# Kernel optimization log

Measured on AMD Instinct MI355X. Metric: run time of the kernel, lower is better.

## Reference

```python
import jax, jax.numpy as jnp
import numpy as np

MIN_NORM = 1e-15
PROJ_EPS = 4e-3   # HGCN fp32 boundary eps
C = 1.0           # curvature (args.c)
SQRT_C = 1.0
LOOP_ATT = 10.0   # self-loop weight


def _norm(x):
    return jnp.clip(jnp.linalg.norm(x, axis=-1, keepdims=True), MIN_NORM)


def artanh(x):
    x = jnp.clip(x, -1.0 + 1e-6, 1.0 - 1e-6)
    return 0.5 * (jnp.log1p(x) - jnp.log1p(-x))


def proj(x):
    # project back inside the Poincare ball
    n = _norm(x)
    maxn = (1.0 - PROJ_EPS) / SQRT_C
    return jnp.where(n > maxn, x / n * maxn, x)


def expmap0(u):
    n = _norm(u)
    return jnp.tanh(SQRT_C * n) * u / (SQRT_C * n)


def logmap0(p):
    n = _norm(p)
    return artanh(SQRT_C * n) * p / (SQRT_C * n)


def mobius_add(x, y):
    x2 = jnp.sum(x * x, -1, keepdims=True)
    y2 = jnp.sum(y * y, -1, keepdims=True)
    xy = jnp.sum(x * y, -1, keepdims=True)
    num = (1.0 + 2.0 * C * xy + C * y2) * x + (1.0 - C * x2) * y
    den = 1.0 + 2.0 * C * xy + C * C * x2 * y2
    return num / jnp.clip(den, MIN_NORM)


def mobius_matvec(W, x):
    xn = _norm(x)
    mx = x @ W.T                       # [N, out]
    mxn = _norm(mx)
    res = jnp.tanh(mxn / xn * artanh(SQRT_C * xn)) * mx / (mxn * SQRT_C)
    zero = jnp.all(mx == 0, axis=-1, keepdims=True)
    return jnp.where(zero, 0.0, res)


def normalize_adj(adj):
    # symmetric D^{-1/2} A D^{-1/2}
    deg = jnp.sum(adj, axis=-1)
    dinv = jnp.where(deg > 0, deg ** -0.5, 0.0)
    return dinv[:, None] * adj * dinv[None, :]


def encode(x, adj, W_stack, b_stack):
    # map features onto the manifold: proj(expmap0(proj_tan0(x))) ; proj_tan0 = id
    h = proj(expmap0(x))
    for i in range(W_stack.shape[0]):
        # HypLinear: mobius matvec + hyperbolic bias add
        m = proj(mobius_matvec(W_stack[i], h))
        hb = proj(expmap0(b_stack[i][None, :]))
        m = proj(mobius_add(m, hb))
        # HypAgg: aggregate in tangent space at origin
        m = proj(expmap0(adj @ logmap0(m)))
        # HypAct: relu in tangent space
        h = proj(expmap0(jax.nn.relu(logmap0(m))))
    return h


def readout(h):
    # cat(global_avg_pool, global_max_pool) over nodes -> [2*d]
    return jnp.concatenate([jnp.mean(h, axis=0), jnp.max(h, axis=0)])


def setup_inputs() -> dict:
    key = jax.random.key(0)
    ks = jax.random.split(key, 12)
    N, F, D, L = 4096, 128, 128, 2
    x1 = jax.random.normal(ks[0], (1, N, F), jnp.float32)
    x2 = jax.random.normal(ks[1], (1, N, F), jnp.float32)
    adj1 = jax.random.uniform(ks[2], (1, N, N), dtype=jnp.float32)
    adj2 = jax.random.uniform(ks[3], (1, N, N), dtype=jnp.float32)
    dist1 = jax.random.uniform(ks[4], (N, N), dtype=jnp.float32)
    dist2 = jax.random.uniform(ks[5], (N, N), dtype=jnp.float32)
    W_stack = jax.random.normal(ks[6], (L, D, F), jnp.float32) * 0.05
    b_stack = jax.random.normal(ks[7], (L, D), jnp.float32) * 0.01
    W_mlp1 = jax.random.normal(ks[8], (D, 6 * D), jnp.float32) * 0.05
    b_mlp1 = jnp.zeros((D,), jnp.float32)
    W_mlp2 = jax.random.normal(ks[9], (1, D), jnp.float32) * 0.05
    b_mlp2 = jnp.zeros((1,), jnp.float32)
    return dict(x1=x1, x2=x2, adj1=adj1, adj2=adj2, dist1=dist1, dist2=dist2,
                W_stack=W_stack, b_stack=b_stack,
                W_mlp1=W_mlp1, b_mlp1=b_mlp1, W_mlp2=W_mlp2, b_mlp2=b_mlp2)


def reference(x1, x2, adj1, adj2, dist1, dist2, W_stack, b_stack,
              W_mlp1, b_mlp1, W_mlp2, b_mlp2):
    N = x1.shape[1]
    eye = jnp.eye(N, dtype=x1.dtype)
    a1 = normalize_adj(adj1[0] + LOOP_ATT * eye)
    a2 = normalize_adj(adj2[0] + LOOP_ATT * eye)
    out1 = encode(x1[0], a1, W_stack, b_stack)
    out2 = encode(x2[0], a2, W_stack, b_stack)
    h1 = readout(out1)
    h2 = readout(out2)
    feat = jnp.concatenate([h1, h2, h1 - h2])            # [6*d]
    hidden = jax.nn.gelu(feat @ W_mlp1.T + b_mlp1, approximate=False)
    logits = hidden @ W_mlp2.T + b_mlp2                  # [1]
    return logits
```

## Files before the change

kernel.cpp:

```cpp
#include <hip/hip_runtime.h>
#include <math.h>

#define MIN_NORM 1e-15f
#define MAXN 0.996f

typedef __attribute__((ext_vector_type(8))) short bf16x8;
typedef __attribute__((ext_vector_type(16))) float f32x16;

union U8 { unsigned short s[8]; bf16x8 v; };

static __device__ __forceinline__ float wsum(float v) {
#pragma unroll
    for (int o = 32; o > 0; o >>= 1) v += __shfl_xor(v, o, 64);
    return v;
}
static __device__ __forceinline__ float artanh_f(float x) {
    const float lim = 1.0f - 1e-6f;
    x = fminf(fmaxf(x, -lim), lim);
    return 0.5f * (log1pf(x) - log1pf(-x));
}

static __device__ __forceinline__ void split3(float a, unsigned short& h,
                                              unsigned short& l, unsigned short& ll) {
    unsigned u = __float_as_uint(a);
    unsigned hb = u & 0xFFFF0000u;
    float r1 = a - __uint_as_float(hb);
    unsigned u1 = __float_as_uint(r1);
    unsigned lb = u1 & 0xFFFF0000u;
    float r2 = r1 - __uint_as_float(lb);
    unsigned u2 = __float_as_uint(r2);
    unsigned t = u2 + 0x7FFFu + ((u2 >> 16) & 1u);
    h = (unsigned short)(hb >> 16);
    l = (unsigned short)(lb >> 16);
    ll = (unsigned short)(t >> 16);
}

__global__ void k_transW_hb(const float* __restrict__ W, float* __restrict__ Wt,
                            const float* __restrict__ b_stack, float* __restrict__ hb) {
    int l = blockIdx.y;
    int t = blockIdx.x * 256 + threadIdx.x;
    int k = t >> 7, d = t & 127;
    Wt[l * 16384 + k * 128 + d] = W[l * 16384 + d * 128 + k];
    if (blockIdx.x == 0 && threadIdx.x < 64) {
        int lane = threadIdx.x;
        float2 b = ((const float2*)(b_stack + l * 128))[lane];
        float n = fmaxf(sqrtf(wsum(b.x * b.x + b.y * b.y)), MIN_NORM);
        float sc = tanhf(n) / n;
        float hx = sc * b.x, hy = sc * b.y;
        float nm = fmaxf(sqrtf(wsum(hx * hx + hy * hy)), MIN_NORM);
        if (nm > MAXN) { float s = MAXN / nm; hx *= s; hy *= s; }
        ((float2*)(hb + l * 128))[lane] = make_float2(hx, hy);
    }
}

__global__ __launch_bounds__(256) void k_deg(const float* __restrict__ adj1,
                                             const float* __restrict__ adj2,
                                             float* __restrict__ dinv) {
    int row = blockIdx.x, g = blockIdx.y;
    const float* adj = (g ? adj2 : adj1) + (size_t)row * 4096;
    float s = 0.f;
    for (int i = threadIdx.x; i < 1024; i += 256) {
        float4 v = ((const float4*)adj)[i];
        s += v.x + v.y + v.z + v.w;
    }
    s = wsum(s);
    __shared__ float ls[4];
    if ((threadIdx.x & 63) == 0) ls[threadIdx.x >> 6] = s;
    __syncthreads();
    if (threadIdx.x == 0) {
        float t = ls[0] + ls[1] + ls[2] + ls[3] + 10.0f;
        dinv[g * 4096 + row] = (t > 0.f) ? (1.0f / sqrtf(t)) : 0.f;
    }
}

__global__ __launch_bounds__(256) void k_manifold(const float* __restrict__ x1,
                                                  const float* __restrict__ x2,
                                                  float* __restrict__ h) {
    int wid = threadIdx.x >> 6, lane = threadIdx.x & 63;
    int row = blockIdx.x * 4 + wid;
    const float* x = (row < 4096 ? x1 : x2 - (size_t)4096 * 128) + (size_t)row * 128;
    float2 v = ((const float2*)x)[lane];
    float n = fmaxf(sqrtf(wsum(v.x * v.x + v.y * v.y)), MIN_NORM);
    float sc = tanhf(n) / n;
    float hx = sc * v.x, hy = sc * v.y;
    float nm = fmaxf(sqrtf(wsum(hx * hx + hy * hy)), MIN_NORM);
    if (nm > MAXN) { float s = MAXN / nm; hx *= s; hy *= s; }
    ((float2*)(h + (size_t)row * 128))[lane] = make_float2(hx, hy);
}

__global__ __launch_bounds__(256) void k_lin(const float* __restrict__ A,
                                             const float* __restrict__ Bt,
                                             float* __restrict__ C) {
    int r0 = blockIdx.x * 64;
    __shared__ float As[32][64];
    __shared__ float Bs[32][128];
    int t = threadIdx.x;
    int tx = t & 15, ty = t >> 4;
    float acc[4][8] = {};
    int ar = t >> 3;
    int ac = (t & 7) * 4;
    for (int kt = 0; kt < 128; kt += 32) {
        const float* Ap = A + (size_t)(r0 + ar) * 128 + kt + ac;
        float4 v0 = *(const float4*)Ap;
        float4 v1 = *(const float4*)(Ap + 32 * 128);
        As[ac + 0][ar] = v0.x; As[ac + 1][ar] = v0.y; As[ac + 2][ar] = v0.z; As[ac + 3][ar] = v0.w;
        As[ac + 0][ar + 32] = v1.x; As[ac + 1][ar + 32] = v1.y; As[ac + 2][ar + 32] = v1.z; As[ac + 3][ar + 32] = v1.w;
#pragma unroll
        for (int i = 0; i < 4; i++) {
            int f = t + 256 * i;
            int kr = f >> 5, c = (f & 31) * 4;
            *(float4*)&Bs[kr][c] = *(const float4*)(Bt + (size_t)(kt + kr) * 128 + c);
        }
        __syncthreads();
#pragma unroll
        for (int k = 0; k < 32; k++) {
            float4 a = *(const float4*)&As[k][ty * 4];
            float4 b0 = *(const float4*)&Bs[k][tx * 4];
            float4 b1 = *(const float4*)&Bs[k][64 + tx * 4];
            float av[4] = {a.x, a.y, a.z, a.w};
            float bv[8] = {b0.x, b0.y, b0.z, b0.w, b1.x, b1.y, b1.z, b1.w};
#pragma unroll
            for (int i = 0; i < 4; i++)
#pragma unroll
                for (int j = 0; j < 8; j++)
                    acc[i][j] = fmaf(av[i], bv[j], acc[i][j]);
        }
        __syncthreads();
    }
#pragma unroll
    for (int i = 0; i < 4; i++) {
        float* Cr = C + (size_t)(r0 + ty * 4 + i) * 128;
        *(float4*)(Cr + tx * 4) = make_float4(acc[i][0], acc[i][1], acc[i][2], acc[i][3]);
        *(float4*)(Cr + 64 + tx * 4) = make_float4(acc[i][4], acc[i][5], acc[i][6], acc[i][7]);
    }
}

__global__ __launch_bounds__(256) void k_postlin(const float* __restrict__ h,
                                                 const float* __restrict__ mx,
                                                 const float* __restrict__ hb,
                                                 const float* __restrict__ dinv,
                                                 float* __restrict__ tp) {
    int wid = threadIdx.x >> 6, lane = threadIdx.x & 63;
    int row = blockIdx.x * 4 + wid;
    float2 hv = ((const float2*)(h + (size_t)row * 128))[lane];
    float2 mv = ((const float2*)(mx + (size_t)row * 128))[lane];
    float xn = fmaxf(sqrtf(wsum(hv.x * hv.x + hv.y * hv.y)), MIN_NORM);
    float mxn = fmaxf(sqrtf(wsum(mv.x * mv.x + mv.y * mv.y)), MIN_NORM);
    float arg = mxn / xn * artanh_f(xn);
    float sc = tanhf(arg) / mxn;
    float rx = sc * mv.x, ry = sc * mv.y;
    float nr = fmaxf(sqrtf(wsum(rx * rx + ry * ry)), MIN_NORM);
    if (nr > MAXN) { float s = MAXN / nr; rx *= s; ry *= s; }
    float2 bv = ((const float2*)hb)[lane];
    float x2 = wsum(rx * rx + ry * ry);
    float y2 = wsum(bv.x * bv.x + bv.y * bv.y);
    float xy = wsum(rx * bv.x + ry * bv.y);
    float cx = 1.0f + 2.0f * xy + y2;
    float cy = 1.0f - x2;
    float den = fmaxf(1.0f + 2.0f * xy + x2 * y2, MIN_NORM);
    float mxo = (cx * rx + cy * bv.x) / den;
    float myo = (cx * ry + cy * bv.y) / den;
    float nm = fmaxf(sqrtf(wsum(mxo * mxo + myo * myo)), MIN_NORM);
    if (nm > MAXN) { float s = MAXN / nm; mxo *= s; myo *= s; }
    float nm2 = fmaxf(sqrtf(wsum(mxo * mxo + myo * myo)), MIN_NORM);
    float lsc = artanh_f(nm2) / nm2;
    float dv = dinv[row];
    ((float2*)(tp + (size_t)row * 128))[lane] =
        make_float2(dv * (lsc * mxo), dv * (lsc * myo));
}

__global__ __launch_bounds__(256) void k_tsplit(const float* __restrict__ tp,
                                                unsigned short* __restrict__ Ph,
                                                unsigned short* __restrict__ Pl,
                                                unsigned short* __restrict__ Pll) {
    __shared__ float L[64][128];
    int g = blockIdx.y;
    int k0 = blockIdx.x * 64;
    const float* T = tp + ((size_t)g * 4096 + k0) * 128;
    int t = threadIdx.x;
#pragma unroll
    for (int i = 0; i < 8; i++) {
        int f = t + 256 * i;
        int r = f >> 5, c4 = f & 31;
        *(float4*)&L[r][c4 * 4] = *(const float4*)(T + (size_t)r * 128 + c4 * 4);
    }
    __syncthreads();
    int c = t & 127, lhi = t >> 7;
    int c31 = c & 31, ct = c >> 5;
#pragma unroll
    for (int q = 0; q < 4; q++) {
        int kb = (k0 >> 4) + q;
        U8 ah, al, al2;
#pragma unroll
        for (int j = 0; j < 8; j++)
            split3(L[q * 16 + lhi * 8 + j][c], ah.s[j], al.s[j], al2.s[j]);
        size_t off = ((((size_t)g * 256 + kb) * 4 + ct) * 64 + lhi * 32 + c31) * 8;
        *(bf16x8*)(Ph + off) = ah.v;
        *(bf16x8*)(Pl + off) = al.v;
        *(bf16x8*)(Pll + off) = al2.v;
    }
}

static __device__ __forceinline__ void step16(const unsigned short Bsc[][512], int cb,
                                              int lane, float4 a0, float4 a1,
                                              f32x16* acc) {
    bf16x8 bh[4], bl[4], bll[4];
#pragma unroll
    for (int ct = 0; ct < 4; ct++) {
        bh[ct]  = *(const bf16x8*)&Bsc[cb + ct][lane * 8];
        bl[ct]  = *(const bf16x8*)&Bsc[cb + 4 + ct][lane * 8];
        bll[ct] = *(const bf16x8*)&Bsc[cb + 8 + ct][lane * 8];
    }
    U8 ah, al, al2;
    float av[8] = {a0.x, a0.y, a0.z, a0.w, a1.x, a1.y, a1.z, a1.w};
#pragma unroll
    for (int j = 0; j < 8; j++) split3(av[j], ah.s[j], al.s[j], al2.s[j]);
#pragma unroll
    for (int ct = 0; ct < 4; ct++)
        acc[ct] = __builtin_amdgcn_mfma_f32_32x32x16_bf16(ah.v, bh[ct], acc[ct], 0, 0, 0);
#pragma unroll
    for (int ct = 0; ct < 4; ct++)
        acc[ct] = __builtin_amdgcn_mfma_f32_32x32x16_bf16(al.v, bh[ct], acc[ct], 0, 0, 0);
#pragma unroll
    for (int ct = 0; ct < 4; ct++)
        acc[ct] = __builtin_amdgcn_mfma_f32_32x32x16_bf16(ah.v, bl[ct], acc[ct], 0, 0, 0);
#pragma unroll
    for (int ct = 0; ct < 4; ct++)
        acc[ct] = __builtin_amdgcn_mfma_f32_32x32x16_bf16(al.v, bl[ct], acc[ct], 0, 0, 0);
#pragma unroll
    for (int ct = 0; ct < 4; ct++)
        acc[ct] = __builtin_amdgcn_mfma_f32_32x32x16_bf16(ah.v, bll[ct], acc[ct], 0, 0, 0);
#pragma unroll
    for (int ct = 0; ct < 4; ct++)
        acc[ct] = __builtin_amdgcn_mfma_f32_32x32x16_bf16(al2.v, bh[ct], acc[ct], 0, 0, 0);
}

__global__ __launch_bounds__(256, 2) void k_agg_mfma(
    const float* __restrict__ adj1, const float* __restrict__ adj2,
    const unsigned short* __restrict__ Ph, const unsigned short* __restrict__ Pl,
    const unsigned short* __restrict__ Pll, float* __restrict__ part) {
    __shared__ __align__(16) unsigned short Bs[2][24][512];
    const int w = threadIdx.x >> 6, lane = threadIdx.x & 63;
    const int mt = blockIdx.x, ks = blockIdx.y, g = blockIdx.z;
    const float* __restrict__ A = g ? adj2 : adj1;
    const int l31 = lane & 31, lhi = lane >> 5;
    const float* Ap = A + (size_t)(mt * 128 + w * 32 + l31) * 4096 + ks * 512 + lhi * 8;

    const unsigned short* src[3];
#pragma unroll
    for (int i = 0; i < 3; i++) {
        int c = w * 3 + i;
        const unsigned short* Pb = (c < 4) ? Ph : ((c < 8) ? Pl : Pll);
        src[i] = Pb + ((((size_t)(g * 256 + ks * 32)) * 4 + (c & 3)) * 64 + lane) * 8;
    }

    f32x16 acc[4] = {};
    float4 a0 = *(const float4*)Ap,        a1 = *(const float4*)(Ap + 4);
    float4 a2 = *(const float4*)(Ap + 16), a3 = *(const float4*)(Ap + 20);

    {
        bf16x8 r0 = *(const bf16x8*)(src[0]);
        bf16x8 r1 = *(const bf16x8*)(src[1]);
        bf16x8 r2 = *(const bf16x8*)(src[2]);
        bf16x8 r3 = *(const bf16x8*)(src[0] + 2048);
        bf16x8 r4 = *(const bf16x8*)(src[1] + 2048);
        bf16x8 r5 = *(const bf16x8*)(src[2] + 2048);
        *(bf16x8*)&Bs[0][w * 3 + 0][lane * 8] = r0;
        *(bf16x8*)&Bs[0][w * 3 + 1][lane * 8] = r1;
        *(bf16x8*)&Bs[0][w * 3 + 2][lane * 8] = r2;
        *(bf16x8*)&Bs[0][12 + w * 3 + 0][lane * 8] = r3;
        *(bf16x8*)&Bs[0][12 + w * 3 + 1][lane * 8] = r4;
        *(bf16x8*)&Bs[0][12 + w * 3 + 2][lane * 8] = r5;
    }
    __syncthreads();

    for (int p = 0; p < 16; p++) {
        const int cur = p & 1;
        const bool more = (p + 1 < 16);
        bf16x8 r0, r1, r2, r3, r4, r5;
        if (more) {
            size_t adv = (size_t)(2 * (p + 1)) * 2048;
            r0 = *(const bf16x8*)(src[0] + adv);
            r1 = *(const bf16x8*)(src[1] + adv);
            r2 = *(const bf16x8*)(src[2] + adv);
            r3 = *(const bf16x8*)(src[0] + adv + 2048);
            r4 = *(const bf16x8*)(src[1] + adv + 2048);
            r5 = *(const bf16x8*)(src[2] + adv + 2048);
        }
        const float* An = more ? (Ap + 32) : Ap;
        float4 n0 = *(const float4*)An,        n1 = *(const float4*)(An + 4);
        float4 n2 = *(const float4*)(An + 16), n3 = *(const float4*)(An + 20);
        Ap += 32;
        step16(Bs[cur], 0,  lane, a0, a1, acc);
        step16(Bs[cur], 12, lane, a2, a3, acc);
        if (more) {
            const int nb = cur ^ 1;
            *(bf16x8*)&Bs[nb][w * 3 + 0][lane * 8] = r0;
            *(bf16x8*)&Bs[nb][w * 3 + 1][lane * 8] = r1;
            *(bf16x8*)&Bs[nb][w * 3 + 2][lane * 8] = r2;
            *(bf16x8*)&Bs[nb][12 + w * 3 + 0][lane * 8] = r3;
            *(bf16x8*)&Bs[nb][12 + w * 3 + 1][lane * 8] = r4;
            *(bf16x8*)&Bs[nb][12 + w * 3 + 2][lane * 8] = r5;
        }
        asm volatile("s_waitcnt lgkmcnt(0)" ::: "memory");
        __builtin_amdgcn_sched_barrier(0);
        __builtin_amdgcn_s_barrier();
        a0 = n0; a1 = n1; a2 = n2; a3 = n3;
    }

    float* P = part + ((size_t)(g * 8 + ks) * 4096) * 128;
    const int rb = mt * 128 + w * 32 + 4 * lhi;
#pragma unroll
    for (int ct = 0; ct < 4; ct++) {
        const int c = ct * 32 + l31;
#pragma unroll
        for (int q = 0; q < 16; q++) {
            int r = rb + (q & 3) + 8 * (q >> 2);
            P[(size_t)r * 128 + c] = acc[ct][q];
        }
    }
}

__global__ __launch_bounds__(256) void k_reduce(const float* __restrict__ part,
                                                const float* __restrict__ tp,
                                                const float* __restrict__ dinv,
                                                float* __restrict__ h) {
    int wid = threadIdx.x >> 6, lane = threadIdx.x & 63;
    int row = blockIdx.x * 4 + wid;
    int g = row >> 12, rr = row & 4095;
    float sx = 0.f, sy = 0.f;
    const float* P = part + ((size_t)(g * 8) * 4096 + rr) * 128;
#pragma unroll
    for (int ks = 0; ks < 8; ks++) {
        float2 v = ((const float2*)(P + (size_t)ks * 4096 * 128))[lane];
        sx += v.x; sy += v.y;
    }
    float2 tv = ((const float2*)(tp + (size_t)row * 128))[lane];
    float d = dinv[row];
    float vx = d * (sx + 10.0f * tv.x);
    float vy = d * (sy + 10.0f * tv.y);
    float n = fmaxf(sqrtf(wsum(vx * vx + vy * vy)), MIN_NORM);
    float e = tanhf(n) / n;
    float px = e * vx, py = e * vy;
    float nm = fmaxf(sqrtf(wsum(px * px + py * py)), MIN_NORM);
    if (nm > MAXN) { float s = MAXN / nm; px *= s; py *= s; }
    float nm2 = fmaxf(sqrtf(wsum(px * px + py * py)), MIN_NORM);
    float lsc = artanh_f(nm2) / nm2;
    float tx2 = fmaxf(lsc * px, 0.0f), ty2 = fmaxf(lsc * py, 0.0f);
    float nr = fmaxf(sqrtf(wsum(tx2 * tx2 + ty2 * ty2)), MIN_NORM);
    float e2 = tanhf(nr) / nr;
    float hx = e2 * tx2, hy = e2 * ty2;
    float nh = fmaxf(sqrtf(wsum(hx * hx + hy * hy)), MIN_NORM);
    if (nh > MAXN) { float s = MAXN / nh; hx *= s; hy *= s; }
    ((float2*)(h + (size_t)row * 128))[lane] = make_float2(hx, hy);
}

__global__ __launch_bounds__(256) void k_red_part(const float* __restrict__ h,
                                                  float* __restrict__ part) {
    int chunk = blockIdx.x;
    int col = threadIdx.x & 127, half = threadIdx.x >> 7;
    float s = 0.f, m = -INFINITY;
    for (int i = 0; i < 64; i++) {
        int r = chunk * 128 + half * 64 + i;
        float v = h[(size_t)r * 128 + col];
        s += v;
        m = fmaxf(m, v);
    }
    __shared__ float ss[128], sm[128];
    if (half) { ss[col] = s; sm[col] = m; }
    __syncthreads();
    if (!half) {
        s += ss[col];
        m = fmaxf(m, sm[col]);
        part[(chunk * 2 + 0) * 128 + col] = s;
        part[(chunk * 2 + 1) * 128 + col] = m;
    }
}

__global__ void k_red_final(const float* __restrict__ part, float* __restrict__ feat) {
    int g = blockIdx.x, col = threadIdx.x;
    float s = 0.f, m = -INFINITY;
    for (int c = g * 32; c < g * 32 + 32; c++) {
        s += part[(c * 2 + 0) * 128 + col];
        m = fmaxf(m, part[(c * 2 + 1) * 128 + col]);
    }
    feat[g * 256 + col] = s * (1.0f / 4096.0f);
    feat[g * 256 + 128 + col] = m;
}

__global__ __launch_bounds__(256) void k_mlp_hidden(const float* __restrict__ feat,
                                                    const float* __restrict__ W1,
                                                    const float* __restrict__ b1,
                                                    float* __restrict__ hidden) {
    int j = blockIdx.x;
    int t = threadIdx.x;
    float p = 0.f;
    for (int k = t; k < 768; k += 256) {
        float f = (k < 512) ? feat[k] : (feat[k - 512] - feat[k - 256]);
        p = fmaf(f, W1[j * 768 + k], p);
    }
    p = wsum(p);
    __shared__ float ps[4];
    if ((t & 63) == 0) ps[t >> 6] = p;
    __syncthreads();
    if (t == 0) {
        float x = ps[0] + ps[1] + ps[2] + ps[3] + b1[j];
        hidden[j] = 0.5f * x * (1.0f + erff(x * 0.70710678118654752f));
    }
}

__global__ void k_mlp_out(const float* __restrict__ hidden, const float* __restrict__ W2,
                          const float* __restrict__ b2, float* __restrict__ out) {
    int t = threadIdx.x;
    float v = hidden[t] * W2[t];
    v = wsum(v);
    __shared__ float ps[2];
    if ((t & 63) == 0) ps[t >> 6] = v;
    __syncthreads();
    if (t == 0) out[0] = ps[0] + ps[1] + b2[0];
}

extern "C" void kernel_launch(void* const* d_in, const int* in_sizes, int n_in,
                              void* d_out, int out_size, void* d_ws, size_t ws_size,
                              hipStream_t stream) {
    (void)in_sizes; (void)n_in; (void)out_size; (void)ws_size;
    const float* x1 = (const float*)d_in[0];
    const float* x2 = (const float*)d_in[1];
    const float* adj1 = (const float*)d_in[2];
    const float* adj2 = (const float*)d_in[3];
    const float* W_stack = (const float*)d_in[6];
    const float* b_stack = (const float*)d_in[7];
    const float* W1 = (const float*)d_in[8];
    const float* b1 = (const float*)d_in[9];
    const float* W2 = (const float*)d_in[10];
    const float* b2 = (const float*)d_in[11];

    float* ws = (float*)d_ws;
    float* dinv = ws;
    float* hb   = ws + 8192;
    float* Wt   = ws + 8448;
    float* h    = ws + 41216;
    float* mx   = h + 1048576;
    float* tp   = mx + 1048576;
    float* part = tp + 1048576;
    float* rpart = part + 8388608;
    float* feat = rpart + 16384;
    float* hid  = feat + 512;
    unsigned short* Ph  = (unsigned short*)(hid + 128);
    unsigned short* Pl  = Ph + 2 * 128 * 4096;
    unsigned short* Pll = Pl + 2 * 128 * 4096;

    k_transW_hb<<<dim3(64, 2), 256, 0, stream>>>(W_stack, Wt, b_stack, hb);
    k_deg<<<dim3(4096, 2), 256, 0, stream>>>(adj1, adj2, dinv);
    k_manifold<<<2048, 256, 0, stream>>>(x1, x2, h);
    for (int l = 0; l < 2; l++) {
        k_lin<<<128, 256, 0, stream>>>(h, Wt + l * 16384, mx);
        k_postlin<<<2048, 256, 0, stream>>>(h, mx, hb + l * 128, dinv, tp);
        k_tsplit<<<dim3(64, 2), 256, 0, stream>>>(tp, Ph, Pl, Pll);
        k_agg_mfma<<<dim3(32, 8, 2), 256, 0, stream>>>(adj1, adj2, Ph, Pl, Pll, part);
        k_reduce<<<2048, 256, 0, stream>>>(part, tp, dinv, h);
    }
    k_red_part<<<64, 256, 0, stream>>>(h, rpart);
    k_red_final<<<2, 128, 0, stream>>>(rpart, feat);
    k_mlp_hidden<<<128, 256, 0, stream>>>(feat, W1, b1, hid);
    k_mlp_out<<<1, 128, 0, stream>>>(hid, W2, b2, (float*)d_out);
}
```

Measured before the change: 212.3 us.

## Double aggregation row tile per block to reuse shared B fragments

```diff
diff --git a/kernel.cpp b/kernel.cpp
--- a/kernel.cpp
+++ b/kernel.cpp
@@ -201,9 +201,10 @@
     }
 }
 
-static __device__ __forceinline__ void step16(const unsigned short Bsc[][512], int cb,
-                                              int lane, float4 a0, float4 a1,
-                                              f32x16* acc) {
+static __device__ __forceinline__ void step16x2(const unsigned short Bsc[][512], int cb,
+                                                int lane, float4 a0, float4 a1,
+                                                float4 c0, float4 c1,
+                                                f32x16* accA, f32x16* accB) {
     bf16x8 bh[4], bl[4], bll[4];
 #pragma unroll
     for (int ct = 0; ct < 4; ct++) {
@@ -211,31 +212,45 @@
         bl[ct]  = *(const bf16x8*)&Bsc[cb + 4 + ct][lane * 8];
         bll[ct] = *(const bf16x8*)&Bsc[cb + 8 + ct][lane * 8];
     }
-    U8 ah, al, al2;
-    float av[8] = {a0.x, a0.y, a0.z, a0.w, a1.x, a1.y, a1.z, a1.w};
-#pragma unroll
-    for (int j = 0; j < 8; j++) split3(av[j], ah.s[j], al.s[j], al2.s[j]);
-#pragma unroll
-    for (int ct = 0; ct < 4; ct++)
-        acc[ct] = __builtin_amdgcn_mfma_f32_32x32x16_bf16(ah.v, bh[ct], acc[ct], 0, 0, 0);
-#pragma unroll
-    for (int ct = 0; ct < 4; ct++)
-        acc[ct] = __builtin_amdgcn_mfma_f32_32x32x16_bf16(al.v, bh[ct], acc[ct], 0, 0, 0);
-#pragma unroll
-    for (int ct = 0; ct < 4; ct++)
-        acc[ct] = __builtin_amdgcn_mfma_f32_32x32x16_bf16(ah.v, bl[ct], acc[ct], 0, 0, 0);
-#pragma unroll
-    for (int ct = 0; ct < 4; ct++)
-        acc[ct] = __builtin_amdgcn_mfma_f32_32x32x16_bf16(al.v, bl[ct], acc[ct], 0, 0, 0);
-#pragma unroll
-    for (int ct = 0; ct < 4; ct++)
-        acc[ct] = __builtin_amdgcn_mfma_f32_32x32x16_bf16(ah.v, bll[ct], acc[ct], 0, 0, 0);
-#pragma unroll
-    for (int ct = 0; ct < 4; ct++)
-        acc[ct] = __builtin_amdgcn_mfma_f32_32x32x16_bf16(al2.v, bh[ct], acc[ct], 0, 0, 0);
-}
-
-__global__ __launch_bounds__(256, 2) void k_agg_mfma(
+    U8 xh, xl, xq, yh, yl, yq;
+    float xa[8] = {a0.x, a0.y, a0.z, a0.w, a1.x, a1.y, a1.z, a1.w};
+    float ya[8] = {c0.x, c0.y, c0.z, c0.w, c1.x, c1.y, c1.z, c1.w};
+#pragma unroll
+    for (int j = 0; j < 8; j++) { split3(xa[j], xh.s[j], xl.s[j], xq.s[j]);
+                                  split3(ya[j], yh.s[j], yl.s[j], yq.s[j]); }
+#pragma unroll
+    for (int ct = 0; ct < 4; ct++) {
+        accA[ct] = __builtin_amdgcn_mfma_f32_32x32x16_bf16(xh.v, bh[ct], accA[ct], 0, 0, 0);
+        accB[ct] = __builtin_amdgcn_mfma_f32_32x32x16_bf16(yh.v, bh[ct], accB[ct], 0, 0, 0);
+    }
+#pragma unroll
+    for (int ct = 0; ct < 4; ct++) {
+        accA[ct] = __builtin_amdgcn_mfma_f32_32x32x16_bf16(xl.v, bh[ct], accA[ct], 0, 0, 0);
+        accB[ct] = __builtin_amdgcn_mfma_f32_32x32x16_bf16(yl.v, bh[ct], accB[ct], 0, 0, 0);
+    }
+#pragma unroll
+    for (int ct = 0; ct < 4; ct++) {
+        accA[ct] = __builtin_amdgcn_mfma_f32_32x32x16_bf16(xh.v, bl[ct], accA[ct], 0, 0, 0);
+        accB[ct] = __builtin_amdgcn_mfma_f32_32x32x16_bf16(yh.v, bl[ct], accB[ct], 0, 0, 0);
+    }
+#pragma unroll
+    for (int ct = 0; ct < 4; ct++) {
+        accA[ct] = __builtin_amdgcn_mfma_f32_32x32x16_bf16(xl.v, bl[ct], accA[ct], 0, 0, 0);
+        accB[ct] = __builtin_amdgcn_mfma_f32_32x32x16_bf16(yl.v, bl[ct], accB[ct], 0, 0, 0);
+    }
+#pragma unroll
+    for (int ct = 0; ct < 4; ct++) {
+        accA[ct] = __builtin_amdgcn_mfma_f32_32x32x16_bf16(xh.v, bll[ct], accA[ct], 0, 0, 0);
+        accB[ct] = __builtin_amdgcn_mfma_f32_32x32x16_bf16(yh.v, bll[ct], accB[ct], 0, 0, 0);
+    }
+#pragma unroll
+    for (int ct = 0; ct < 4; ct++) {
+        accA[ct] = __builtin_amdgcn_mfma_f32_32x32x16_bf16(xq.v, bh[ct], accA[ct], 0, 0, 0);
+        accB[ct] = __builtin_amdgcn_mfma_f32_32x32x16_bf16(yq.v, bh[ct], accB[ct], 0, 0, 0);
+    }
+}
+
+__global__ __launch_bounds__(256, 1) void k_agg_mfma(
     const float* __restrict__ adj1, const float* __restrict__ adj2,
     const unsigned short* __restrict__ Ph, const unsigned short* __restrict__ Pl,
     const unsigned short* __restrict__ Pll, float* __restrict__ part) {
@@ -244,33 +259,38 @@
     const int mt = blockIdx.x, ks = blockIdx.y, g = blockIdx.z;
     const float* __restrict__ A = g ? adj2 : adj1;
     const int l31 = lane & 31, lhi = lane >> 5;
-    const float* Ap = A + (size_t)(mt * 128 + w * 32 + l31) * 4096 + ks * 512 + lhi * 8;
-
-    const unsigned short* src[3];
-#pragma unroll
-    for (int i = 0; i < 3; i++) {
-        int c = w * 3 + i;
-        const unsigned short* Pb = (c < 4) ? Ph : ((c < 8) ? Pl : Pll);
-        src[i] = Pb + ((((size_t)(g * 256 + ks * 32)) * 4 + (c & 3)) * 64 + lane) * 8;
-    }
-
-    f32x16 acc[4] = {};
-    float4 a0 = *(const float4*)Ap,        a1 = *(const float4*)(Ap + 4);
-    float4 a2 = *(const float4*)(Ap + 16), a3 = *(const float4*)(Ap + 20);
+    const float* Ap0 = A + (size_t)(mt * 256 + w * 32 + l31) * 4096 + ks * 512 + lhi * 8;
+    const float* Ap1 = Ap0 + (size_t)128 * 4096;
+
+    const unsigned short* src[6];
+#pragma unroll
+    for (int i = 0; i < 6; i++) {
+        int c = w * 6 + i;
+        int step = (c >= 12) ? 1 : 0;
+        int cc = c - step * 12;
+        const unsigned short* Pb = (cc < 4) ? Ph : ((cc < 8) ? Pl : Pll);
+        src[i] = Pb + ((((size_t)(g * 256 + ks * 32 + step)) * 4 + (cc & 3)) * 64 + lane) * 8;
+    }
+
+    f32x16 accA[4] = {}, accB[4] = {};
+    float4 a0 = *(const float4*)Ap0,        a1 = *(const float4*)(Ap0 + 4);
+    float4 a2 = *(const float4*)(Ap0 + 16), a3 = *(const float4*)(Ap0 + 20);
+    float4 a4 = *(const float4*)Ap1,        a5 = *(const float4*)(Ap1 + 4);
+    float4 a6 = *(const float4*)(Ap1 + 16), a7 = *(const float4*)(Ap1 + 20);
 
     {
         bf16x8 r0 = *(const bf16x8*)(src[0]);
         bf16x8 r1 = *(const bf16x8*)(src[1]);
         bf16x8 r2 = *(const bf16x8*)(src[2]);
-        bf16x8 r3 = *(const bf16x8*)(src[0] + 2048);
-        bf16x8 r4 = *(const bf16x8*)(src[1] + 2048);
-        bf16x8 r5 = *(const bf16x8*)(src[2] + 2048);
-        *(bf16x8*)&Bs[0][w * 3 + 0][lane * 8] = r0;
-        *(bf16x8*)&Bs[0][w * 3 + 1][lane * 8] = r1;
-        *(bf16x8*)&Bs[0][w * 3 + 2][lane * 8] = r2;
-        *(bf16x8*)&Bs[0][12 + w * 3 + 0][lane * 8] = r3;
-        *(bf16x8*)&Bs[0][12 + w * 3 + 1][lane * 8] = r4;
-        *(bf16x8*)&Bs[0][12 + w * 3 + 2][lane * 8] = r5;
+        bf16x8 r3 = *(const bf16x8*)(src[3]);
+        bf16x8 r4 = *(const bf16x8*)(src[4]);
+        bf16x8 r5 = *(const bf16x8*)(src[5]);
+        *(bf16x8*)&Bs[0][w * 6 + 0][lane * 8] = r0;
+        *(bf16x8*)&Bs[0][w * 6 + 1][lane * 8] = r1;
+        *(bf16x8*)&Bs[0][w * 6 + 2][lane * 8] = r2;
+        *(bf16x8*)&Bs[0][w * 6 + 3][lane * 8] = r3;
+        *(bf16x8*)&Bs[0][w * 6 + 4][lane * 8] = r4;
+        *(bf16x8*)&Bs[0][w * 6 + 5][lane * 8] = r5;
     }
     __syncthreads();
 
@@ -279,44 +299,49 @@
         const bool more = (p + 1 < 16);
         bf16x8 r0, r1, r2, r3, r4, r5;
         if (more) {
-            size_t adv = (size_t)(2 * (p + 1)) * 2048;
+            size_t adv = (size_t)(p + 1) * 4096;
             r0 = *(const bf16x8*)(src[0] + adv);
             r1 = *(const bf16x8*)(src[1] + adv);
             r2 = *(const bf16x8*)(src[2] + adv);
-            r3 = *(const bf16x8*)(src[0] + adv + 2048);
-            r4 = *(const bf16x8*)(src[1] + adv + 2048);
-            r5 = *(const bf16x8*)(src[2] + adv + 2048);
+            r3 = *(const bf16x8*)(src[3] + adv);
+            r4 = *(const bf16x8*)(src[4] + adv);
+            r5 = *(const bf16x8*)(src[5] + adv);
         }
-        const float* An = more ? (Ap + 32) : Ap;
-        float4 n0 = *(const float4*)An,        n1 = *(const float4*)(An + 4);
-        float4 n2 = *(const float4*)(An + 16), n3 = *(const float4*)(An + 20);
-        Ap += 32;
-        step16(Bs[cur], 0,  lane, a0, a1, acc);
-        step16(Bs[cur], 12, lane, a2, a3, acc);
+        const float* An0 = more ? (Ap0 + 32) : Ap0;
+        const float* An1 = more ? (Ap1 + 32) : Ap1;
+        float4 n0 = *(const float4*)An0,        n1 = *(const float4*)(An0 + 4);
+        float4 n2 = *(const float4*)(An0 + 16), n3 = *(const float4*)(An0 + 20);
+        float4 n4 = *(const float4*)An1,        n5 = *(const float4*)(An1 + 4);
+        float4 n6 = *(const float4*)(An1 + 16), n7 = *(const float4*)(An1 + 20);
+        Ap0 += 32; Ap1 += 32;
+        step16x2(Bs[cur], 0,  lane, a0, a1, a4, a5, accA, accB);
+        step16x2(Bs[cur], 12, lane, a2, a3, a6, a7, accA, accB);
         if (more) {
             const int nb = cur ^ 1;
-            *(bf16x8*)&Bs[nb][w * 3 + 0][lane * 8] = r0;
-            *(bf16x8*)&Bs[nb][w * 3 + 1][lane * 8] = r1;
-            *(bf16x8*)&Bs[nb][w * 3 + 2][lane * 8] = r2;
-            *(bf16x8*)&Bs[nb][12 + w * 3 + 0][lane * 8] = r3;
-            *(bf16x8*)&Bs[nb][12 + w * 3 + 1][lane * 8] = r4;
-            *(bf16x8*)&Bs[nb][12 + w * 3 + 2][lane * 8] = r5;
+            *(bf16x8*)&Bs[nb][w * 6 + 0][lane * 8] = r0;
+            *(bf16x8*)&Bs[nb][w * 6 + 1][lane * 8] = r1;
+            *(bf16x8*)&Bs[nb][w * 6 + 2][lane * 8] = r2;
+            *(bf16x8*)&Bs[nb][w * 6 + 3][lane * 8] = r3;
+            *(bf16x8*)&Bs[nb][w * 6 + 4][lane * 8] = r4;
+            *(bf16x8*)&Bs[nb][w * 6 + 5][lane * 8] = r5;
         }
         asm volatile("s_waitcnt lgkmcnt(0)" ::: "memory");
         __builtin_amdgcn_sched_barrier(0);
         __builtin_amdgcn_s_barrier();
         a0 = n0; a1 = n1; a2 = n2; a3 = n3;
+        a4 = n4; a5 = n5; a6 = n6; a7 = n7;
     }
 
     float* P = part + ((size_t)(g * 8 + ks) * 4096) * 128;
-    const int rb = mt * 128 + w * 32 + 4 * lhi;
+    const int rb0 = mt * 256 + w * 32 + 4 * lhi;
 #pragma unroll
     for (int ct = 0; ct < 4; ct++) {
         const int c = ct * 32 + l31;
 #pragma unroll
         for (int q = 0; q < 16; q++) {
-            int r = rb + (q & 3) + 8 * (q >> 2);
-            P[(size_t)r * 128 + c] = acc[ct][q];
+            int dr = (q & 3) + 8 * (q >> 2);
+            P[(size_t)(rb0 + dr) * 128 + c] = accA[ct][q];
+            P[(size_t)(rb0 + 128 + dr) * 128 + c] = accB[ct][q];
         }
     }
 }
@@ -457,7 +482,7 @@
         k_lin<<<128, 256, 0, stream>>>(h, Wt + l * 16384, mx);
         k_postlin<<<2048, 256, 0, stream>>>(h, mx, hb + l * 128, dinv, tp);
         k_tsplit<<<dim3(64, 2), 256, 0, stream>>>(tp, Ph, Pl, Pll);
-        k_agg_mfma<<<dim3(32, 8, 2), 256, 0, stream>>>(adj1, adj2, Ph, Pl, Pll, part);
+        k_agg_mfma<<<dim3(16, 8, 2), 256, 0, stream>>>(adj1, adj2, Ph, Pl, Pll, part);
         k_reduce<<<2048, 256, 0, stream>>>(part, tp, dinv, h);
     }
     k_red_part<<<64, 256, 0, stream>>>(h, rpart);
```

After: 224.0 us. 5.5% more time.
